# Kernel tuning notes

Hardware: AMD Instinct MI355X
Metric: run time of the kernel (lower is better)

The kernel has to match this reference:

```python
import jax, jax.numpy as jnp
import numpy as np

MODEL_DIM = 1024
NUM_HEAD = 16
HEAD_DIM = MODEL_DIM // NUM_HEAD
B, S = 2, 2048


def setup_inputs() -> dict:
    key = jax.random.key(0)
    ks = jax.random.split(key, 13)
    s = 1.0 / np.sqrt(MODEL_DIM)
    inp = {
        "q": jax.random.normal(ks[0], (B, S, MODEL_DIM), jnp.float32),
        "k": jax.random.normal(ks[1], (B, S, MODEL_DIM), jnp.float32),
        "v": jax.random.normal(ks[2], (B, S, MODEL_DIM), jnp.float32),
        "mask": jax.random.randint(ks[3], (S, S), 0, 2, jnp.int32),
        "w_q": jax.random.normal(ks[4], (MODEL_DIM, MODEL_DIM), jnp.float32) * s,
        "b_q": jax.random.normal(ks[5], (MODEL_DIM,), jnp.float32) * s,
        "w_k": jax.random.normal(ks[6], (MODEL_DIM, MODEL_DIM), jnp.float32) * s,
        "b_k": jax.random.normal(ks[7], (MODEL_DIM,), jnp.float32) * s,
        "w_v": jax.random.normal(ks[8], (MODEL_DIM, MODEL_DIM), jnp.float32) * s,
        "b_v": jax.random.normal(ks[9], (MODEL_DIM,), jnp.float32) * s,
        "w_o": jax.random.normal(ks[10], (MODEL_DIM, MODEL_DIM), jnp.float32) * s,
        "b_o": jax.random.normal(ks[11], (MODEL_DIM,), jnp.float32) * s,
    }
    return inp


def reference(q, k, v, mask, w_q, b_q, w_k, b_k, w_v, b_v, w_o, b_o):
    batch, seq_len, dim = q.shape
    # Linear projections (weights stored as [d_in, d_out])
    Q = q @ w_q + b_q
    K = k @ w_k + b_k
    V = v @ w_v + b_v
    # [B, H, S, Dh]
    Q = Q.reshape(batch, seq_len, NUM_HEAD, HEAD_DIM).transpose(0, 2, 1, 3)
    K = K.reshape(batch, seq_len, NUM_HEAD, HEAD_DIM).transpose(0, 2, 1, 3)
    V = V.reshape(batch, seq_len, NUM_HEAD, HEAD_DIM).transpose(0, 2, 1, 3)
    scores = jnp.einsum("bhqd,bhkd->bhqk", Q, K) / jnp.sqrt(
        jnp.asarray(HEAD_DIM, Q.dtype)
    )
    scores = jnp.where(mask == 0, jnp.asarray(-1e9, scores.dtype), scores)
    attn = jax.nn.softmax(scores, axis=-1)
    out = jnp.einsum("bhqk,bhkd->bhqd", attn, V)
    out = out.transpose(0, 2, 1, 3).reshape(batch, seq_len, dim)
    return out @ w_o + b_o
```

## Files before the change

### kernel.cpp

```cpp
#include <hip/hip_runtime.h>
#include <stdint.h>

typedef __bf16 bf16;
typedef __attribute__((ext_vector_type(4))) __bf16 bf16x4;
typedef __attribute__((ext_vector_type(8))) __bf16 bf16x8;
typedef __attribute__((ext_vector_type(4))) float f32x4;
typedef __attribute__((ext_vector_type(2))) float f32x2;

constexpr int S = 2048;
constexpr int D = 1024;
constexpr int H = 16;
constexpr int DH = 64;
constexpr int M = 4096;

constexpr float QSCALE = 0.18033688011112042f;

__device__ __forceinline__ void async16(void* lds, const void* g) {
  __builtin_amdgcn_global_load_lds(
      (const __attribute__((address_space(1))) void*)g,
      (__attribute__((address_space(3))) void*)lds, 16, 0, 0);
}

__global__ __launch_bounds__(256) void prep(
    const int* __restrict__ mask, uint64_t* __restrict__ MB,
    const float* __restrict__ q, const float* __restrict__ k,
    const float* __restrict__ v, bf16* __restrict__ qA, bf16* __restrict__ kA,
    bf16* __restrict__ vA, const float* __restrict__ Wq,
    const float* __restrict__ Wk, const float* __restrict__ Wv,
    const float* __restrict__ Wo, bf16* __restrict__ WTq,
    bf16* __restrict__ WTk, bf16* __restrict__ WTv, bf16* __restrict__ WoTh,
    bf16* __restrict__ WoTl) {
  __shared__ float T[64 * 68];
  const int bid = blockIdx.x;
  const int tid = threadIdx.x;

  if (bid < 16384) {
    const int gid = bid * 4 + (tid >> 6);
    const int lane = tid & 63;
    const int kt = gid >> 11;
    const int qq = gid & (S - 1);
    int mv = mask[(size_t)qq * S + kt * 64 + lane];
    uint64_t bits = __ballot(mv != 0);
    if (lane == 0) MB[(size_t)kt * S + qq] = bits;
    return;
  }

  if (bid < 28672) {
    const int idx = bid - 16384;
    const int z = idx >> 12;
    const int x = idx & 4095;
    const float* src = (z == 0) ? q : (z == 1) ? k : v;
    bf16* dst = (z == 0) ? qA : (z == 1) ? kA : vA;
    const size_t i = ((size_t)x * 256 + tid) * 4;
    f32x4 xv = *(const f32x4*)(src + i);
    bf16x4 o;
#pragma unroll
    for (int j = 0; j < 4; j++) o[j] = (bf16)xv[j];
    *(bf16x4*)(dst + i) = o;
    return;
  }

  const int idx = bid - 28672;
  const int z = idx >> 8;
  const int xy = idx & 255;
  const int n0 = (xy >> 4) * 64, k0 = (xy & 15) * 64;
  const float* W = (z == 0) ? Wq : (z == 1) ? Wk : (z == 2) ? Wv : Wo;
  const int lr = tid >> 4, lc = (tid & 15) * 4;
#pragma unroll
  for (int r = 0; r < 4; r++) {
    f32x4 vv = *(const f32x4*)(W + (size_t)(k0 + r * 16 + lr) * 1024 + n0 + lc);
    *(f32x4*)&T[(r * 16 + lr) * 68 + lc] = vv;
  }
  __syncthreads();
  const int nn = tid >> 3, kc = (tid & 7) * 8;
#pragma unroll
  for (int p = 0; p < 2; p++) {
    int n = p * 32 + nn;
    bf16x8 h, l;
#pragma unroll
    for (int j = 0; j < 8; j++) {
      float vv = T[(kc + j) * 68 + n];
      bf16 hh = (bf16)vv;
      h[j] = hh;
      l[j] = (bf16)(vv - (float)hh);
    }
    if (z < 3) {
      bf16* WT = (z == 0) ? WTq : (z == 1) ? WTk : WTv;
      *(bf16x8*)(WT + (size_t)(n0 + n) * 1024 + k0 + kc) = h;
    } else {
      *(bf16x8*)(WoTh + (size_t)(n0 + n) * 1024 + k0 + kc) = h;
      *(bf16x8*)(WoTl + (size_t)(n0 + n) * 1024 + k0 + kc) = l;
    }
  }
}

__global__ __launch_bounds__(256) void gemm_qkv(
    const bf16* __restrict__ Aq, const bf16* __restrict__ Ak,
    const bf16* __restrict__ Av, const bf16* __restrict__ WTq,
    const bf16* __restrict__ WTk, const bf16* __restrict__ WTv,
    const float* __restrict__ bq, const float* __restrict__ bk,
    const float* __restrict__ bv, bf16* __restrict__ Qb,
    bf16* __restrict__ Kb, bf16* __restrict__ VT) {
  __shared__ char smem[34816];

  const int z = blockIdx.z;
  const bf16* A = (z == 0) ? Aq : (z == 1) ? Ak : Av;
  const bf16* WT = (z == 0) ? WTq : (z == 1) ? WTk : WTv;
  const float* bias = (z == 0) ? bq : (z == 1) ? bk : bv;
  const float oscale = (z == 0) ? QSCALE : 1.0f;

  const int tid = threadIdx.x;
  const int bn = blockIdx.x * 128;
  const int bm = blockIdx.y * 128;
  const int wv = tid >> 6;
  const int lane = tid & 63;
  const int quad = lane >> 4;
  const int lo = lane & 15;
  const int wm = (wv >> 1) * 64;
  const int wn = (wv & 1) * 64;

  f32x4 acc[4][4];
#pragma unroll
  for (int i = 0; i < 4; i++)
#pragma unroll
    for (int j = 0; j < 4; j++) acc[i][j] = {0.f, 0.f, 0.f, 0.f};

  const int rloc = lane >> 3;
  const int gx = (lane & 7) ^ rloc;
  const int rx = (lo & 7);

  for (int kt = 0; kt < 16; ++kt) {
#pragma unroll
    for (int j = 0; j < 4; j++) {
      int ch = wv * 4 + j;
      async16(smem + ch * 1024,
              A + (size_t)(bm + ch * 8 + rloc) * 1024 + kt * 64 + gx * 8);
      async16(smem + 16384 + ch * 1024,
              WT + (size_t)(bn + ch * 8 + rloc) * 1024 + kt * 64 + gx * 8);
    }
    __syncthreads();

#pragma unroll
    for (int ks = 0; ks < 2; ks++) {
      bf16x8 af[4], bfr[4];
#pragma unroll
      for (int mi = 0; mi < 4; mi++)
        af[mi] = *(const bf16x8*)(smem + (wm + mi * 16 + lo) * 128 +
                                  (((ks * 4 + quad) ^ rx) * 16));
#pragma unroll
      for (int ni = 0; ni < 4; ni++)
        bfr[ni] = *(const bf16x8*)(smem + 16384 + (wn + ni * 16 + lo) * 128 +
                                   (((ks * 4 + quad) ^ rx) * 16));
#pragma unroll
      for (int mi = 0; mi < 4; mi++)
#pragma unroll
        for (int ni = 0; ni < 4; ni++)
          acc[mi][ni] = __builtin_amdgcn_mfma_f32_16x16x32_bf16(
              af[mi], bfr[ni], acc[mi][ni], 0, 0, 0);
    }
    __syncthreads();
  }

  const int b = bm >> 11;
  const int srow0 = bm & (S - 1);

  if (z == 2) {
#pragma unroll
    for (int mi = 0; mi < 4; mi++)
#pragma unroll
      for (int ni = 0; ni < 4; ni++) {
        int col = bn + wn + ni * 16 + lo;
        int h = col >> 6, dh = col & 63;
        float bvv = bias[col];
        bf16x4 t;
#pragma unroll
        for (int r = 0; r < 4; r++) t[r] = (bf16)(acc[mi][ni][r] + bvv);
        int s0 = srow0 + wm + mi * 16 + quad * 4;
        *(bf16x4*)&VT[(((size_t)(b * H + h)) * DH + dh) * S + s0] = t;
      }
    return;
  }

  bf16* T = (bf16*)smem;
#pragma unroll
  for (int mi = 0; mi < 4; mi++)
#pragma unroll
    for (int ni = 0; ni < 4; ni++) {
      int col = wn + ni * 16 + lo;
      float bvv = bias[bn + col];
#pragma unroll
      for (int r = 0; r < 4; r++) {
        int row = wm + mi * 16 + quad * 4 + r;
        T[row * 136 + col] = (bf16)((acc[mi][ni][r] + bvv) * oscale);
      }
    }
  __syncthreads();
  bf16* out = (z == 0) ? Qb : Kb;
  const int rr = tid >> 1;
  const int half = tid & 1;
  const int h = (bn >> 6) + half;
  bf16* gp = out + (((size_t)(b * H + h)) * S + srow0 + rr) * DH;
#pragma unroll
  for (int j = 0; j < 8; j++)
    *(bf16x8*)(gp + j * 8) = *(const bf16x8*)&T[rr * 136 + half * 64 + j * 8];
}

__global__ __launch_bounds__(512) void gemm_o(
    const bf16* __restrict__ AOh, const bf16* __restrict__ AOl,
    const bf16* __restrict__ Wh, const bf16* __restrict__ Wl,
    const float* __restrict__ bias, float* __restrict__ out) {
  __shared__ char smem[32768];

  const int tid = threadIdx.x;
  const int bn = blockIdx.x * 128;
  const int bm = blockIdx.y * 128;
  const int wv = tid >> 6;
  const int lane = tid & 63;
  const int quad = lane >> 4;
  const int lo = lane & 15;
  const int wm = (wv >> 1) * 32;
  const int wn = (wv & 1) * 64;

  f32x4 acc[2][4];
#pragma unroll
  for (int i = 0; i < 2; i++)
#pragma unroll
    for (int j = 0; j < 4; j++) acc[i][j] = {0.f, 0.f, 0.f, 0.f};

  const int pl = lane >> 3;
  const int uu = lane & 7;
  const int srow = pl * 2 + (uu & 1);
  const int sg = (uu >> 1) ^ (pl & 3);
  const int uread = (((quad ^ ((lo >> 1) & 3)) << 1) | (lo & 1)) * 16;
  const int aoff = (lo >> 1) * 128 + uread;

  for (int kt = 0; kt < 32; ++kt) {
#pragma unroll
    for (int t = 0; t < 4; t++) {
      const bf16* src = (t == 0) ? AOh : (t == 1) ? AOl : (t == 2) ? Wh : Wl;
      int rb = (t < 2) ? bm : bn;
      async16(smem + t * 8192 + wv * 1024,
              src + (size_t)(rb + wv * 16 + srow) * 1024 + kt * 32 + sg * 8);
    }
    __syncthreads();

    bf16x8 ah[2], al[2], bh[4], bl[4];
    const char* ap = smem + wm * 64 + aoff;
    const char* bp = smem + 16384 + wn * 64 + aoff;
#pragma unroll
    for (int mi = 0; mi < 2; mi++) {
      ah[mi] = *(const bf16x8*)(ap + mi * 1024);
      al[mi] = *(const bf16x8*)(ap + 8192 + mi * 1024);
    }
#pragma unroll
    for (int ni = 0; ni < 4; ni++) {
      bh[ni] = *(const bf16x8*)(bp + ni * 1024);
      bl[ni] = *(const bf16x8*)(bp + 8192 + ni * 1024);
    }
#pragma unroll
    for (int mi = 0; mi < 2; mi++)
#pragma unroll
      for (int ni = 0; ni < 4; ni++) {
        acc[mi][ni] = __builtin_amdgcn_mfma_f32_16x16x32_bf16(ah[mi], bh[ni], acc[mi][ni], 0, 0, 0);
        acc[mi][ni] = __builtin_amdgcn_mfma_f32_16x16x32_bf16(ah[mi], bl[ni], acc[mi][ni], 0, 0, 0);
        acc[mi][ni] = __builtin_amdgcn_mfma_f32_16x16x32_bf16(al[mi], bh[ni], acc[mi][ni], 0, 0, 0);
      }
    __syncthreads();
  }

#pragma unroll
  for (int mi = 0; mi < 2; mi++)
#pragma unroll
    for (int ni = 0; ni < 4; ni++) {
      int col = bn + wn + ni * 16 + lo;
      float bvv = bias[col];
#pragma unroll
      for (int r = 0; r < 4; r++) {
        int row = bm + wm + mi * 16 + quad * 4 + r;
        out[(size_t)row * 1024 + col] = acc[mi][ni][r] + bvv;
      }
    }
}

__global__ __launch_bounds__(512) void attn_kernel(
    const bf16* __restrict__ Qg, const bf16* __restrict__ Kg,
    const bf16* __restrict__ VTg, const uint64_t* __restrict__ MB,
    bf16* __restrict__ AOh, bf16* __restrict__ AOl) {
  __shared__ char smem[49152];

  const int tid = threadIdx.x;
  const int wv = tid >> 6;
  const int lane = tid & 63;
  const int quad = lane >> 4;
  const int lo = lane & 15;

  const int lin = blockIdx.x;
  const int bh = (lin & 7) * 4 + ((lin >> 3) & 3);
  const int qt = lin >> 5;
  const int qbase = qt * 128 + wv * 16;
  const size_t base = (size_t)bh * S * DH;
  bf16* Pw = (bf16*)(smem + 32768 + wv * 2048);
  const int xm = (lo & 7) << 1;

  const int c0 = wv * 2;
  const int rloc = lane >> 3;
  const int gx = (lane & 7) ^ rloc;
  const int rx = lo & 7;

  bf16x8 qf[2];
  {
    const bf16* qp = Qg + base + (size_t)(qbase + lo) * DH + quad * 8;
    qf[0] = *(const bf16x8*)qp;
    qf[1] = *(const bf16x8*)(qp + 32);
  }

  f32x4 Oacc[4];
#pragma unroll
  for (int j = 0; j < 4; j++) Oacc[j] = {0.f, 0.f, 0.f, 0.f};
  f32x2 lp = {0.f, 0.f};

#define STAGE(kt_, buf_)                                                       \
  {                                                                            \
    _Pragma("unroll") for (int j = 0; j < 2; j++) {                            \
      int c = c0 + j;                                                          \
      if (c < 8) {                                                             \
        async16((buf_) + c * 1024,                                             \
                Kg + base + (size_t)((kt_)*64 + c * 8 + rloc) * 64 + gx * 8);  \
      } else {                                                                 \
        int cv = c - 8;                                                        \
        async16((buf_) + 8192 + cv * 1024,                                     \
                VTg + base + (size_t)(cv * 8 + rloc) * S + (kt_)*64 + gx * 8); \
      }                                                                        \
    }                                                                          \
  }

  STAGE(0, smem);
  uint64_t mcur = MB[(size_t)0 * S + qbase + lo];

  for (int kt = 0; kt < 32; ++kt) {
    const char* cur = smem + (kt & 1) * 16384;

    uint64_t m0 = mcur >> (quad * 4);
    uint32_t mw[2] = {(uint32_t)m0, (uint32_t)(m0 >> 32)};

    __syncthreads();
    if (kt + 1 < 32) {
      STAGE(kt + 1, smem + ((kt + 1) & 1) * 16384);
      mcur = MB[(size_t)(kt + 1) * S + qbase + lo];
    }

    const char* Kls = cur;
    const char* Vls = cur + 8192;

    f32x4 sacc[4];
#pragma unroll
    for (int mi = 0; mi < 4; mi++) sacc[mi] = {0.f, 0.f, 0.f, 0.f};
    __builtin_amdgcn_s_setprio(1);
#pragma unroll
    for (int mi = 0; mi < 4; mi++) {
      bf16x8 k0 = *(const bf16x8*)(Kls + (mi * 16 + lo) * 128 + ((quad ^ rx) * 16));
      bf16x8 k1 = *(const bf16x8*)(Kls + (mi * 16 + lo) * 128 + (((4 + quad) ^ rx) * 16));
      sacc[mi] = __builtin_amdgcn_mfma_f32_16x16x32_bf16(k0, qf[0], sacc[mi], 0, 0, 0);
      sacc[mi] = __builtin_amdgcn_mfma_f32_16x16x32_bf16(k1, qf[1], sacc[mi], 0, 0, 0);
    }
    __builtin_amdgcn_s_setprio(0);

#pragma unroll
    for (int mi = 0; mi < 4; mi++) {
      bf16x4 t;
#pragma unroll
      for (int r = 0; r < 4; r++) {
        float p = __builtin_amdgcn_exp2f(sacc[mi][r]);
        int ext = __builtin_amdgcn_sbfe((int)mw[mi >> 1], ((mi & 1) << 4) + r, 1);
        p = __builtin_bit_cast(float, __builtin_bit_cast(int, p) & ext);
        lp[r & 1] += p;
        t[r] = (bf16)p;
      }
      *(bf16x4*)&Pw[lo * 64 + (((mi * 4 + quad) ^ xm) * 4)] = t;
    }

    __builtin_amdgcn_s_setprio(1);
#pragma unroll
    for (int kk = 0; kk < 2; kk++) {
      int g16 = kk * 8 + quad * 2;
      bf16x8 pa = *(const bf16x8*)&Pw[lo * 64 + ((g16 ^ xm) * 4)];
#pragma unroll
      for (int ni = 0; ni < 4; ni++) {
        bf16x8 vb = *(const bf16x8*)(Vls + (ni * 16 + lo) * 128 +
                                     (((kk * 4 + quad) ^ rx) * 16));
        Oacc[ni] = __builtin_amdgcn_mfma_f32_16x16x32_bf16(pa, vb, Oacc[ni], 0, 0, 0);
      }
    }
    __builtin_amdgcn_s_setprio(0);
  }
#undef STAGE

  float lpart = lp[0] + lp[1];
  lpart += __shfl_xor(lpart, 16);
  lpart += __shfl_xor(lpart, 32);

  const int b = bh >> 4, h = bh & (H - 1);
#pragma unroll
  for (int r = 0; r < 4; r++) {
    float inv = 1.0f / __shfl(lpart, quad * 4 + r);
    int q = qbase + quad * 4 + r;
    size_t rowoff = (size_t)(b * S + q) * D + h * DH;
#pragma unroll
    for (int ni = 0; ni < 4; ni++) {
      float o = Oacc[ni][r] * inv;
      bf16 hi = (bf16)o;
      AOh[rowoff + ni * 16 + lo] = hi;
      AOl[rowoff + ni * 16 + lo] = (bf16)(o - (float)hi);
    }
  }
}

extern "C" void kernel_launch(void* const* d_in, const int* in_sizes, int n_in,
                              void* d_out, int out_size, void* d_ws,
                              size_t ws_size, hipStream_t stream) {
  const float* q = (const float*)d_in[0];
  const float* k = (const float*)d_in[1];
  const float* v = (const float*)d_in[2];
  const int* mask = (const int*)d_in[3];
  const float* w_q = (const float*)d_in[4];
  const float* b_q = (const float*)d_in[5];
  const float* w_k = (const float*)d_in[6];
  const float* b_k = (const float*)d_in[7];
  const float* w_v = (const float*)d_in[8];
  const float* b_v = (const float*)d_in[9];
  const float* w_o = (const float*)d_in[10];
  const float* b_o = (const float*)d_in[11];

  char* w = (char*)d_ws;
  const size_t MiB = 1ull << 20;
  bf16* Qb = (bf16*)w;
  bf16* Kb = (bf16*)(w + 8 * MiB);
  bf16* VT = (bf16*)(w + 16 * MiB);
  bf16* qA = (bf16*)(w + 24 * MiB);
  bf16* kA = (bf16*)(w + 32 * MiB);
  bf16* vA = (bf16*)(w + 40 * MiB);
  bf16* AOh = (bf16*)(w + 24 * MiB);
  bf16* AOl = (bf16*)(w + 32 * MiB);
  bf16* WTq = (bf16*)(w + 48 * MiB);
  bf16* WTk = (bf16*)(w + 50 * MiB);
  bf16* WTv = (bf16*)(w + 52 * MiB);
  bf16* WoTh = (bf16*)(w + 54 * MiB);
  bf16* WoTl = (bf16*)(w + 56 * MiB);
  uint64_t* MBits = (uint64_t*)(w + 58 * MiB);

  prep<<<29696, 256, 0, stream>>>(mask, MBits, q, k, v, qA, kA, vA, w_q, w_k,
                                  w_v, w_o, WTq, WTk, WTv, WoTh, WoTl);
  gemm_qkv<<<dim3(8, 32, 3), 256, 0, stream>>>(qA, kA, vA, WTq, WTk, WTv, b_q,
                                               b_k, b_v, Qb, Kb, VT);
  attn_kernel<<<dim3(512), 512, 0, stream>>>(Qb, Kb, VT, MBits, AOh, AOl);
  gemm_o<<<dim3(8, 32), 512, 0, stream>>>(AOh, AOl, WoTh, WoTl, b_o,
                                          (float*)d_out);
}
```

Before: 275.1 us.

## Compute softmax row sums via MFMA with ones vector and coarsen prep blocks

The attention kernel no longer accumulates the softmax denominator with per-element VALU adds plus cross-lane shuffles. Instead it issues one extra MFMA per k-chunk that multiplies the bf16 P tile by a vector of ones, so the row sums land in accumulator registers laid out like the output. Separately, the prep kernel's mask-bit and input-cast phases now process several items per block in unrolled loops, cutting the grid from about 29.7k blocks to 5120. Summing the bf16-rounded probabilities makes the denominator consistent with the numerator, at the cost of extra matrix-unit work in the inner loop.

Result: no change. 280.5 us (+2.0%).

```diff
diff --git a/kernel.cpp b/kernel.cpp
--- a/kernel.cpp
+++ b/kernel.cpp
@@ -5,7 +5,7 @@
 typedef __attribute__((ext_vector_type(4))) __bf16 bf16x4;
 typedef __attribute__((ext_vector_type(8))) __bf16 bf16x8;
 typedef __attribute__((ext_vector_type(4))) float f32x4;
-typedef __attribute__((ext_vector_type(2))) float f32x2;
+typedef __attribute__((ext_vector_type(4))) unsigned int u32x4;
 
 constexpr int S = 2048;
 constexpr int D = 1024;
@@ -34,33 +34,39 @@
   const int bid = blockIdx.x;
   const int tid = threadIdx.x;
 
-  if (bid < 16384) {
-    const int gid = bid * 4 + (tid >> 6);
+  if (bid < 2048) {
+    const int widx = tid >> 6;
     const int lane = tid & 63;
-    const int kt = gid >> 11;
-    const int qq = gid & (S - 1);
-    int mv = mask[(size_t)qq * S + kt * 64 + lane];
-    uint64_t bits = __ballot(mv != 0);
-    if (lane == 0) MB[(size_t)kt * S + qq] = bits;
+#pragma unroll
+    for (int it = 0; it < 8; ++it) {
+      const int gid = (bid * 4 + widx) + it * 8192;
+      const int kt = gid >> 11;
+      const int qq = gid & (S - 1);
+      int mv = mask[(size_t)qq * S + kt * 64 + lane];
+      uint64_t bits = __ballot(mv != 0);
+      if (lane == 0) MB[(size_t)kt * S + qq] = bits;
+    }
     return;
   }
 
-  if (bid < 28672) {
-    const int idx = bid - 16384;
-    const int z = idx >> 12;
-    const int x = idx & 4095;
-    const float* src = (z == 0) ? q : (z == 1) ? k : v;
-    bf16* dst = (z == 0) ? qA : (z == 1) ? kA : vA;
-    const size_t i = ((size_t)x * 256 + tid) * 4;
-    f32x4 xv = *(const f32x4*)(src + i);
-    bf16x4 o;
-#pragma unroll
-    for (int j = 0; j < 4; j++) o[j] = (bf16)xv[j];
-    *(bf16x4*)(dst + i) = o;
+  if (bid < 4096) {
+    size_t t = (size_t)(bid - 2048) * 256 + tid;
+#pragma unroll
+    for (int it = 0; it < 6; ++it, t += 524288) {
+      const int z = (int)(t >> 20);
+      const size_t off = (t & 1048575) * 4;
+      const float* src = (z == 0) ? q : (z == 1) ? k : v;
+      bf16* dst = (z == 0) ? qA : (z == 1) ? kA : vA;
+      f32x4 xv = *(const f32x4*)(src + off);
+      bf16x4 o;
+#pragma unroll
+      for (int j = 0; j < 4; j++) o[j] = (bf16)xv[j];
+      *(bf16x4*)(dst + off) = o;
+    }
     return;
   }
 
-  const int idx = bid - 28672;
+  const int idx = bid - 4096;
   const int z = idx >> 8;
   const int xy = idx & 255;
   const int n0 = (xy >> 4) * 64, k0 = (xy & 15) * 64;
@@ -314,10 +320,13 @@
     qf[1] = *(const bf16x8*)(qp + 32);
   }
 
+  const u32x4 onesw = {0x3F803F80u, 0x3F803F80u, 0x3F803F80u, 0x3F803F80u};
+  const bf16x8 vones = __builtin_bit_cast(bf16x8, onesw);
+
   f32x4 Oacc[4];
 #pragma unroll
   for (int j = 0; j < 4; j++) Oacc[j] = {0.f, 0.f, 0.f, 0.f};
-  f32x2 lp = {0.f, 0.f};
+  f32x4 Osum = {0.f, 0.f, 0.f, 0.f};
 
 #define STAGE(kt_, buf_)                                                       \
   {                                                                            \
@@ -373,7 +382,6 @@
         float p = __builtin_amdgcn_exp2f(sacc[mi][r]);
         int ext = __builtin_amdgcn_sbfe((int)mw[mi >> 1], ((mi & 1) << 4) + r, 1);
         p = __builtin_bit_cast(float, __builtin_bit_cast(int, p) & ext);
-        lp[r & 1] += p;
         t[r] = (bf16)p;
       }
       *(bf16x4*)&Pw[lo * 64 + (((mi * 4 + quad) ^ xm) * 4)] = t;
@@ -390,19 +398,16 @@
                                      (((kk * 4 + quad) ^ rx) * 16));
         Oacc[ni] = __builtin_amdgcn_mfma_f32_16x16x32_bf16(pa, vb, Oacc[ni], 0, 0, 0);
       }
+      Osum = __builtin_amdgcn_mfma_f32_16x16x32_bf16(pa, vones, Osum, 0, 0, 0);
     }
     __builtin_amdgcn_s_setprio(0);
   }
 #undef STAGE
 
-  float lpart = lp[0] + lp[1];
-  lpart += __shfl_xor(lpart, 16);
-  lpart += __shfl_xor(lpart, 32);
-
   const int b = bh >> 4, h = bh & (H - 1);
 #pragma unroll
   for (int r = 0; r < 4; r++) {
-    float inv = 1.0f / __shfl(lpart, quad * 4 + r);
+    float inv = 1.0f / Osum[r];
     int q = qbase + quad * 4 + r;
     size_t rowoff = (size_t)(b * S + q) * D + h * DH;
 #pragma unroll
@@ -448,8 +453,8 @@
   bf16* WoTl = (bf16*)(w + 56 * MiB);
   uint64_t* MBits = (uint64_t*)(w + 58 * MiB);
 
-  prep<<<29696, 256, 0, stream>>>(mask, MBits, q, k, v, qA, kA, vA, w_q, w_k,
-                                  w_v, w_o, WTq, WTk, WTv, WoTh, WoTl);
+  prep<<<5120, 256, 0, stream>>>(mask, MBits, q, k, v, qA, kA, vA, w_q, w_k,
+                                 w_v, w_o, WTq, WTk, WTv, WoTh, WoTl);
   gemm_qkv<<<dim3(8, 32, 3), 256, 0, stream>>>(qA, kA, vA, WTq, WTk, WTv, b_q,
                                                b_k, b_v, Qb, Kb, VT);
   attn_kernel<<<dim3(512), 512, 0, stream>>>(Qb, Kb, VT, MBits, AOh, AOl);
```

## Replace split-bf16 output projection with single fp16 GEMM

Applied to the files above, without the earlier changes.

The output projection previously kept extra precision by splitting the attention output and Wo into bf16 hi/lo pairs and issuing three MFMAs per product. Both operands are now stored as a single fp16 array and multiplied with one fp16 MFMA per tile. The gemm_o kernel is restructured to 256 threads with 64x64 warp tiles, K steps of 64 and an XOR-swizzled LDS layout. This cuts MFMA work and memory traffic for the hi/lo halves, but relies on fp16's 10-bit mantissa being accurate enough, with some risk of tolerance failures or range issues.

Result: faster. 254.5 us (-7.5%).

```diff
diff --git a/kernel.cpp b/kernel.cpp
--- a/kernel.cpp
+++ b/kernel.cpp
@@ -2,8 +2,10 @@
 #include <stdint.h>
 
 typedef __bf16 bf16;
+typedef _Float16 f16;
 typedef __attribute__((ext_vector_type(4))) __bf16 bf16x4;
 typedef __attribute__((ext_vector_type(8))) __bf16 bf16x8;
+typedef __attribute__((ext_vector_type(8))) _Float16 f16x8;
 typedef __attribute__((ext_vector_type(4))) float f32x4;
 typedef __attribute__((ext_vector_type(2))) float f32x2;
 
@@ -28,8 +30,7 @@
     bf16* __restrict__ vA, const float* __restrict__ Wq,
     const float* __restrict__ Wk, const float* __restrict__ Wv,
     const float* __restrict__ Wo, bf16* __restrict__ WTq,
-    bf16* __restrict__ WTk, bf16* __restrict__ WTv, bf16* __restrict__ WoTh,
-    bf16* __restrict__ WoTl) {
+    bf16* __restrict__ WTk, bf16* __restrict__ WTv, f16* __restrict__ WoT) {
   __shared__ float T[64 * 68];
   const int bid = blockIdx.x;
   const int tid = threadIdx.x;
@@ -76,20 +77,17 @@
 #pragma unroll
   for (int p = 0; p < 2; p++) {
     int n = p * 32 + nn;
-    bf16x8 h, l;
-#pragma unroll
-    for (int j = 0; j < 8; j++) {
-      float vv = T[(kc + j) * 68 + n];
-      bf16 hh = (bf16)vv;
-      h[j] = hh;
-      l[j] = (bf16)(vv - (float)hh);
-    }
     if (z < 3) {
+      bf16x8 h;
+#pragma unroll
+      for (int j = 0; j < 8; j++) h[j] = (bf16)T[(kc + j) * 68 + n];
       bf16* WT = (z == 0) ? WTq : (z == 1) ? WTk : WTv;
       *(bf16x8*)(WT + (size_t)(n0 + n) * 1024 + k0 + kc) = h;
     } else {
-      *(bf16x8*)(WoTh + (size_t)(n0 + n) * 1024 + k0 + kc) = h;
-      *(bf16x8*)(WoTl + (size_t)(n0 + n) * 1024 + k0 + kc) = l;
+      f16x8 hf;
+#pragma unroll
+      for (int j = 0; j < 8; j++) hf[j] = (f16)T[(kc + j) * 68 + n];
+      *(f16x8*)(WoT + (size_t)(n0 + n) * 1024 + k0 + kc) = hf;
     }
   }
 }
@@ -205,9 +203,8 @@
     *(bf16x8*)(gp + j * 8) = *(const bf16x8*)&T[rr * 136 + half * 64 + j * 8];
 }
 
-__global__ __launch_bounds__(512) void gemm_o(
-    const bf16* __restrict__ AOh, const bf16* __restrict__ AOl,
-    const bf16* __restrict__ Wh, const bf16* __restrict__ Wl,
+__global__ __launch_bounds__(256) void gemm_o(
+    const f16* __restrict__ A, const f16* __restrict__ WT,
     const float* __restrict__ bias, float* __restrict__ out) {
   __shared__ char smem[32768];
 
@@ -218,58 +215,53 @@
   const int lane = tid & 63;
   const int quad = lane >> 4;
   const int lo = lane & 15;
-  const int wm = (wv >> 1) * 32;
+  const int wm = (wv >> 1) * 64;
   const int wn = (wv & 1) * 64;
 
-  f32x4 acc[2][4];
-#pragma unroll
-  for (int i = 0; i < 2; i++)
+  f32x4 acc[4][4];
+#pragma unroll
+  for (int i = 0; i < 4; i++)
 #pragma unroll
     for (int j = 0; j < 4; j++) acc[i][j] = {0.f, 0.f, 0.f, 0.f};
 
-  const int pl = lane >> 3;
-  const int uu = lane & 7;
-  const int srow = pl * 2 + (uu & 1);
-  const int sg = (uu >> 1) ^ (pl & 3);
-  const int uread = (((quad ^ ((lo >> 1) & 3)) << 1) | (lo & 1)) * 16;
-  const int aoff = (lo >> 1) * 128 + uread;
-
-  for (int kt = 0; kt < 32; ++kt) {
-#pragma unroll
-    for (int t = 0; t < 4; t++) {
-      const bf16* src = (t == 0) ? AOh : (t == 1) ? AOl : (t == 2) ? Wh : Wl;
-      int rb = (t < 2) ? bm : bn;
-      async16(smem + t * 8192 + wv * 1024,
-              src + (size_t)(rb + wv * 16 + srow) * 1024 + kt * 32 + sg * 8);
+  const int rloc = lane >> 3;
+  const int gx = (lane & 7) ^ rloc;
+  const int rx = (lo & 7);
+
+  for (int kt = 0; kt < 16; ++kt) {
+#pragma unroll
+    for (int j = 0; j < 4; j++) {
+      int ch = wv * 4 + j;
+      async16(smem + ch * 1024,
+              A + (size_t)(bm + ch * 8 + rloc) * 1024 + kt * 64 + gx * 8);
+      async16(smem + 16384 + ch * 1024,
+              WT + (size_t)(bn + ch * 8 + rloc) * 1024 + kt * 64 + gx * 8);
     }
     __syncthreads();
 
-    bf16x8 ah[2], al[2], bh[4], bl[4];
-    const char* ap = smem + wm * 64 + aoff;
-    const char* bp = smem + 16384 + wn * 64 + aoff;
-#pragma unroll
-    for (int mi = 0; mi < 2; mi++) {
-      ah[mi] = *(const bf16x8*)(ap + mi * 1024);
-      al[mi] = *(const bf16x8*)(ap + 8192 + mi * 1024);
-    }
-#pragma unroll
-    for (int ni = 0; ni < 4; ni++) {
-      bh[ni] = *(const bf16x8*)(bp + ni * 1024);
-      bl[ni] = *(const bf16x8*)(bp + 8192 + ni * 1024);
-    }
-#pragma unroll
-    for (int mi = 0; mi < 2; mi++)
-#pragma unroll
-      for (int ni = 0; ni < 4; ni++) {
-        acc[mi][ni] = __builtin_amdgcn_mfma_f32_16x16x32_bf16(ah[mi], bh[ni], acc[mi][ni], 0, 0, 0);
-        acc[mi][ni] = __builtin_amdgcn_mfma_f32_16x16x32_bf16(ah[mi], bl[ni], acc[mi][ni], 0, 0, 0);
-        acc[mi][ni] = __builtin_amdgcn_mfma_f32_16x16x32_bf16(al[mi], bh[ni], acc[mi][ni], 0, 0, 0);
-      }
+#pragma unroll
+    for (int ks = 0; ks < 2; ks++) {
+      f16x8 af[4], bfr[4];
+#pragma unroll
+      for (int mi = 0; mi < 4; mi++)
+        af[mi] = *(const f16x8*)(smem + (wm + mi * 16 + lo) * 128 +
+                                 (((ks * 4 + quad) ^ rx) * 16));
+#pragma unroll
+      for (int ni = 0; ni < 4; ni++)
+        bfr[ni] = *(const f16x8*)(smem + 16384 + (wn + ni * 16 + lo) * 128 +
+                                  (((ks * 4 + quad) ^ rx) * 16));
+#pragma unroll
+      for (int mi = 0; mi < 4; mi++)
+#pragma unroll
+        for (int ni = 0; ni < 4; ni++)
+          acc[mi][ni] = __builtin_amdgcn_mfma_f32_16x16x32_f16(
+              af[mi], bfr[ni], acc[mi][ni], 0, 0, 0);
+    }
     __syncthreads();
   }
 
 #pragma unroll
-  for (int mi = 0; mi < 2; mi++)
+  for (int mi = 0; mi < 4; mi++)
 #pragma unroll
     for (int ni = 0; ni < 4; ni++) {
       int col = bn + wn + ni * 16 + lo;
@@ -285,7 +277,7 @@
 __global__ __launch_bounds__(512) void attn_kernel(
     const bf16* __restrict__ Qg, const bf16* __restrict__ Kg,
     const bf16* __restrict__ VTg, const uint64_t* __restrict__ MB,
-    bf16* __restrict__ AOh, bf16* __restrict__ AOl) {
+    f16* __restrict__ AO) {
   __shared__ char smem[49152];
 
   const int tid = threadIdx.x;
@@ -406,12 +398,8 @@
     int q = qbase + quad * 4 + r;
     size_t rowoff = (size_t)(b * S + q) * D + h * DH;
 #pragma unroll
-    for (int ni = 0; ni < 4; ni++) {
-      float o = Oacc[ni][r] * inv;
-      bf16 hi = (bf16)o;
-      AOh[rowoff + ni * 16 + lo] = hi;
-      AOl[rowoff + ni * 16 + lo] = (bf16)(o - (float)hi);
-    }
+    for (int ni = 0; ni < 4; ni++)
+      AO[rowoff + ni * 16 + lo] = (f16)(Oacc[ni][r] * inv);
   }
 }
 
@@ -439,20 +427,17 @@
   bf16* qA = (bf16*)(w + 24 * MiB);
   bf16* kA = (bf16*)(w + 32 * MiB);
   bf16* vA = (bf16*)(w + 40 * MiB);
-  bf16* AOh = (bf16*)(w + 24 * MiB);
-  bf16* AOl = (bf16*)(w + 32 * MiB);
+  f16* AO = (f16*)(w + 24 * MiB);
   bf16* WTq = (bf16*)(w + 48 * MiB);
   bf16* WTk = (bf16*)(w + 50 * MiB);
   bf16* WTv = (bf16*)(w + 52 * MiB);
-  bf16* WoTh = (bf16*)(w + 54 * MiB);
-  bf16* WoTl = (bf16*)(w + 56 * MiB);
+  f16* WoT = (f16*)(w + 54 * MiB);
   uint64_t* MBits = (uint64_t*)(w + 58 * MiB);
 
   prep<<<29696, 256, 0, stream>>>(mask, MBits, q, k, v, qA, kA, vA, w_q, w_k,
-                                  w_v, w_o, WTq, WTk, WTv, WoTh, WoTl);
+                                  w_v, w_o, WTq, WTk, WTv, WoT);
   gemm_qkv<<<dim3(8, 32, 3), 256, 0, stream>>>(qA, kA, vA, WTq, WTk, WTv, b_q,
                                                b_k, b_v, Qb, Kb, VT);
-  attn_kernel<<<dim3(512), 512, 0, stream>>>(Qb, Kb, VT, MBits, AOh, AOl);
-  gemm_o<<<dim3(8, 32), 512, 0, stream>>>(AOh, AOl, WoTh, WoTl, b_o,
-                                          (float*)d_out);
-}
+  attn_kernel<<<dim3(512), 512, 0, stream>>>(Qb, Kb, VT, MBits, AO);
+  gemm_o<<<dim3(8, 32), 256, 0, stream>>>(AO, WoT, b_o, (float*)d_out);
+}
```
